# Kernel tuning notes

Hardware: AMD Instinct MI355X
Metric: run time of the kernel (lower is better)

## Reference

```python
import jax, jax.numpy as jnp
import numpy as np

B, N, K, D = 4096, 64, 48, 64   # batch, n_features, n_bins, d_embedding
F = N * D                        # flattened embedding dim
E, H, O = 8, 1024, 512           # experts, expert hidden, expert out
T, TH = 2, 256                   # tasks, tower hidden


def setup_inputs() -> dict:
    key = jax.random.key(0)
    ks = jax.random.split(key, 10)
    # PLE buffers from uniform bins linspace(0,1,K+1): w = 1/width, b = -edge/width
    edges = jnp.linspace(0.0, 1.0, K + 1)
    width = jnp.diff(edges)
    w = 1.0 / width                      # (K,)
    b = -edges[:-1] / width              # (K,)
    ple_weight = jnp.broadcast_to(w, (N, K)).astype(jnp.float32)
    ple_bias = jnp.broadcast_to(b, (N, K)).astype(jnp.float32)
    s = lambda fan_in: fan_in ** -0.5
    return {
        "x": jax.random.uniform(ks[0], (B, N), jnp.float32),
        "ple_weight": ple_weight,
        "ple_bias": ple_bias,
        "emb_W": jax.random.normal(ks[1], (N, K, D), jnp.float32) * s(K),
        "emb_b": jax.random.normal(ks[2], (N, D), jnp.float32) * s(K),
        "gate_W": jax.random.normal(ks[3], (F, E), jnp.float32) * s(F),
        "gate_b": jnp.zeros((E,), jnp.float32),
        "e_W1": jax.random.normal(ks[4], (E, F, H), jnp.float32) * s(F),
        "e_b1": jnp.zeros((E, H), jnp.float32),
        "e_W2": jax.random.normal(ks[5], (E, H, O), jnp.float32) * s(H),
        "e_b2": jnp.zeros((E, O), jnp.float32),
        "tw1": jax.random.normal(ks[6], (T, O, TH), jnp.float32) * s(O),
        "tb1": jnp.zeros((T, TH), jnp.float32),
        "tw2": jax.random.normal(ks[7], (T, TH, 1), jnp.float32) * s(TH),
        "tb2": jnp.zeros((T, 1), jnp.float32),
        "top_k": 2,
    }


def reference(x, ple_weight, ple_bias, emb_W, emb_b, gate_W, gate_b,
              e_W1, e_b1, e_W2, e_b2, tw1, tb1, tw2, tb2, top_k):
    # --- Piecewise Linear Encoding: (B, N) -> (B, N, K) ---
    enc = ple_bias + ple_weight * x[..., None]
    enc = jnp.concatenate([
        jnp.minimum(enc[..., :1], 1.0),
        jnp.clip(enc[..., 1:-1], 0.0, 1.0),
        jnp.maximum(enc[..., -1:], 0.0),
    ], axis=-1)
    # --- PLE embeddings via NLinear + ReLU: (B, N, K) -> (B, N, D) ---
    emb = jax.nn.relu(jnp.einsum("bnk,nkd->bnd", enc, emb_W) + emb_b)
    flat = emb.reshape(emb.shape[0], -1)                 # (B, F)
    # --- Sparse MoE gating (softmax + top-k renormalized) ---
    probs = jax.nn.softmax(flat @ gate_W + gate_b, axis=-1)   # (B, E)
    topv, topi = jax.lax.top_k(probs, top_k)
    topv = topv / jnp.sum(topv, axis=-1, keepdims=True)
    gates = jnp.zeros_like(probs).at[jnp.arange(probs.shape[0])[:, None], topi].set(topv)
    # --- Experts (computed densely, gated combine) ---
    h = jax.nn.relu(jnp.einsum("bf,efh->beh", flat, e_W1) + e_b1)   # (B, E, H)
    eo = jnp.einsum("beh,eho->beo", h, e_W2) + e_b2                 # (B, E, O)
    moe = jnp.einsum("be,beo->bo", gates, eo)                       # (B, O)
    # --- Task towers: per-task MLP -> scalar ---
    th = jax.nn.relu(jnp.einsum("bo,tos->bts", moe, tw1) + tb1)     # (B, T, TH)
    out = (jnp.einsum("bts,tsu->btu", th, tw2) + tb2)[..., 0]       # (B, T)
    return out
```

## Files before the change

### kernel.cpp

```cpp
#include <hip/hip_runtime.h>
#include <cstdint>

#define B_ 4096
#define N_ 64
#define K_ 48
#define D_ 64
#define F_ 4096
#define E_ 8
#define H_ 1024
#define O_ 512
#define T_ 2
#define TH_ 256
#define NSLOT (B_ * 2)

#define MAXT1 72

typedef float f32x4 __attribute__((ext_vector_type(4)));
typedef __bf16 bf16x8 __attribute__((ext_vector_type(8)));

__device__ __forceinline__ unsigned short f2bf(float f) {
    union { float f; unsigned int u; } v; v.f = f;
    unsigned int u = v.u;
    u += 0x7FFFu + ((u >> 16) & 1u);
    return (unsigned short)(u >> 16);
}

__device__ __forceinline__ void gload_lds16(const void* gptr, void* lptr) {
    auto* g = reinterpret_cast<const __attribute__((address_space(1))) unsigned int*>(
        reinterpret_cast<uintptr_t>(gptr));
    auto* l = reinterpret_cast<__attribute__((address_space(3))) unsigned int*>(
        reinterpret_cast<uintptr_t>(lptr));
    __builtin_amdgcn_global_load_lds(g, l, 16, 0, 0);
}

__global__ __launch_bounds__(64) void prefix_kernel(
    const float* __restrict__ embW, const float* __restrict__ embB,
    float* __restrict__ P)
{
    int n = blockIdx.x;
    int lane = threadIdx.x;
    float acc = embB[n * D_ + lane];
    const float* wsrc = embW + (size_t)n * K_ * D_ + lane;
    float* dst = P + (size_t)n * K_ * D_ + lane;
    #pragma unroll 8
    for (int k = 0; k < K_; ++k) {
        dst[k * D_] = acc;
        acc += wsrc[k * D_];
    }
}

__global__ __launch_bounds__(256) void ple_embed_kernel(
    const float* __restrict__ x, const float* __restrict__ plw,
    const float* __restrict__ plb, const float* __restrict__ embW,
    const float* __restrict__ P, const float* __restrict__ gateW,
    unsigned short* __restrict__ flat_bf, float* __restrict__ logits)
{
    __shared__ float gpart[4][E_];
    int b = blockIdx.x;
    int tid = threadIdx.x, lane = tid & 63, w = tid >> 6;

    float xl = x[b * N_ + lane];
    float gp[E_];
    #pragma unroll
    for (int e = 0; e < E_; ++e) gp[e] = 0.0f;

    #pragma unroll 4
    for (int i = 0; i < 16; ++i) {
        int n = w * 16 + i;
        float xn = __shfl(xl, n);
        const float* pw = plw + n * K_;
        const float* pb = plb + n * K_;
        float t = fmaf(pw[0], xn, pb[0]);
        int j = (int)t;
        j = max(0, min(K_ - 1, j));
        float f = fminf(fmaxf(fmaf(pw[j], xn, pb[j]), 0.0f), 1.0f);
        size_t base = ((size_t)n * K_ + j) * D_ + lane;
        float emb = fmaxf(fmaf(f, embW[base], P[base]), 0.0f);
        flat_bf[(size_t)b * F_ + n * D_ + lane] = f2bf(emb);

        const float4* gw4 = (const float4*)(gateW + (size_t)(n * D_ + lane) * E_);
        float4 g0 = gw4[0], g1 = gw4[1];
        gp[0] = fmaf(emb, g0.x, gp[0]);
        gp[1] = fmaf(emb, g0.y, gp[1]);
        gp[2] = fmaf(emb, g0.z, gp[2]);
        gp[3] = fmaf(emb, g0.w, gp[3]);
        gp[4] = fmaf(emb, g1.x, gp[4]);
        gp[5] = fmaf(emb, g1.y, gp[5]);
        gp[6] = fmaf(emb, g1.z, gp[6]);
        gp[7] = fmaf(emb, g1.w, gp[7]);
    }

    #pragma unroll
    for (int off = 32; off > 0; off >>= 1) {
        #pragma unroll
        for (int e = 0; e < E_; ++e) gp[e] += __shfl_down(gp[e], off);
    }
    if (lane == 0) {
        #pragma unroll
        for (int e = 0; e < E_; ++e) gpart[w][e] = gp[e];
    }
    __syncthreads();
    if (tid < E_)
        logits[b * E_ + tid] =
            gpart[0][tid] + gpart[1][tid] + gpart[2][tid] + gpart[3][tid];
}

__global__ __launch_bounds__(256) void gate_top2_kernel(
    const float* __restrict__ logits, const float* __restrict__ gate_b,
    int* __restrict__ topi, float* __restrict__ topg, int* __restrict__ counts)
{
    int b = blockIdx.x * 256 + threadIdx.x;
    int lane = threadIdx.x & 63;
    float l[E_];
    #pragma unroll
    for (int e = 0; e < E_; ++e) l[e] = logits[b * E_ + e] + gate_b[e];
    int e1 = 0; float v1 = l[0];
    #pragma unroll
    for (int e = 1; e < E_; ++e) if (l[e] > v1) { v1 = l[e]; e1 = e; }
    int e2 = -1; float v2 = -1e30f;
    #pragma unroll
    for (int e = 0; e < E_; ++e) if (e != e1 && l[e] > v2) { v2 = l[e]; e2 = e; }
    float ex = expf(v2 - v1);
    float g1 = 1.0f / (1.0f + ex);
    float g2 = ex / (1.0f + ex);
    topi[b * 2] = e1; topi[b * 2 + 1] = e2;
    topg[b * 2] = g1; topg[b * 2 + 1] = g2;
    #pragma unroll
    for (int e = 0; e < E_; ++e) {
        unsigned long long m1 = __ballot(e1 == e);
        unsigned long long m2 = __ballot(e2 == e);
        if (lane == 0) {
            int c = __popcll(m1) + __popcll(m2);
            if (c) atomicAdd(&counts[e], c);
        }
    }
}

__global__ void scan_kernel(const int* __restrict__ counts, int* __restrict__ offsets,
                            int* __restrict__ tiles1, int* __restrict__ ntiles) {
    int e = threadIdx.x;
    if (e >= E_) return;
    int c[E_];
    #pragma unroll
    for (int i = 0; i < E_; ++i) c[i] = counts[i];
    int off = 0, tb = 0, tot = 0, ttot = 0;
    #pragma unroll
    for (int i = 0; i < E_; ++i) {
        int t = (c[i] + 127) >> 7;
        if (i < e) { off += c[i]; tb += t; }
        tot += c[i]; ttot += t;
    }
    offsets[e] = off;
    if (e == 0) { offsets[E_] = tot; ntiles[0] = ttot; }
    int nt = (c[e] + 127) >> 7;
    for (int tr = 0; tr < nt; ++tr) tiles1[tb + tr] = (e << 16) | tr;
}

__global__ __launch_bounds__(256) void scatter_kernel(
    const int* __restrict__ topi, const float* __restrict__ topg,
    const int* __restrict__ offsets, int* __restrict__ cursors,
    int* __restrict__ rows, float* __restrict__ gatev, int* __restrict__ slots)
{
    int b = blockIdx.x * 256 + threadIdx.x;
    int lane = threadIdx.x & 63;
    #pragma unroll
    for (int j = 0; j < 2; ++j) {
        int e = topi[b * 2 + j];
        float g = topg[b * 2 + j];
        #pragma unroll
        for (int ex = 0; ex < E_; ++ex) {
            unsigned long long m = __ballot(e == ex);
            if (e == ex) {
                int leader = __builtin_ctzll(m);
                int base = 0;
                if (lane == leader) base = atomicAdd(&cursors[ex], __popcll(m));
                base = __shfl(base, leader);
                int pos = base + __popcll(m & ((1ull << lane) - 1ull));
                int slot = offsets[ex] + pos;
                rows[slot] = b;
                gatev[slot] = g;
                slots[b * 2 + j] = slot;
            }
        }
    }
}

__global__ __launch_bounds__(256) void wfrag_kernel(
    const float* __restrict__ in, unsigned short* __restrict__ out, int R, int C)
{
    __shared__ float tile[64][65];
    int e = blockIdx.z;
    int rb = blockIdx.x, cb = blockIdx.y;
    const float* src = in + (size_t)e * R * C + (size_t)(rb * 64) * C + cb * 64;
    int lane = threadIdx.x & 63, w = threadIdx.x >> 6;
    #pragma unroll
    for (int i = 0; i < 16; ++i) {
        int r = w * 16 + i;
        tile[r][lane] = src[(size_t)r * C + lane];
    }
    __syncthreads();
    int NB = C >> 4, KB = R >> 5;
    #pragma unroll
    for (int it = 0; it < 2; ++it) {
        int t = threadIdx.x + it * 256;
        int n0r = t >> 7, k0r = (t >> 6) & 1, ln = t & 63;
        int q = ln >> 4, nl = ln & 15;
        unsigned short v[8];
        #pragma unroll
        for (int j = 0; j < 8; ++j)
            v[j] = f2bf(tile[k0r * 32 + q * 8 + j][n0r * 16 + nl]);
        size_t didx = (((size_t)e * NB + cb * 4 + n0r) * KB + rb * 2 + k0r) * 512
                      + (size_t)ln * 8;
        uint4 pk;
        pk.x = v[0] | ((unsigned)v[1] << 16);
        pk.y = v[2] | ((unsigned)v[3] << 16);
        pk.z = v[4] | ((unsigned)v[5] << 16);
        pk.w = v[6] | ((unsigned)v[7] << 16);
        *(uint4*)&out[didx] = pk;
    }
}

__global__ __launch_bounds__(256) void fc1_kernel(
    const unsigned short* __restrict__ Abf,
    const unsigned short* __restrict__ Wf,
    const float* __restrict__ bias,
    const int* __restrict__ rows, const int* __restrict__ offsets,
    const int* __restrict__ tiles1, const int* __restrict__ ntiles,
    unsigned short* __restrict__ Hbf)
{
    int bid = blockIdx.x;
    int tlow = bid & 7;
    int rest = bid >> 3;
    int cn   = rest & 15;
    int tile = (rest >> 4) * 8 + tlow;
    if (tile >= ntiles[0]) return;
    int te = tiles1[tile];
    int e = te >> 16, tr = te & 0xffff;
    int m0 = offsets[e], mEnd = offsets[e + 1];
    int Me = mEnd - m0;

    __shared__ alignas(16) unsigned short As[2][128 * 64];

    int tid = threadIdx.x, lane = tid & 63, wv = tid >> 6;
    int lr = lane >> 3;
    int cg = (lane & 7) ^ lr;

    const unsigned short* aptr[4];
    #pragma unroll
    for (int i = 0; i < 4; ++i) {
        int rowA = (wv * 4 + i) * 8 + lr;
        int slot = min(m0 + tr * 128 + rowA, mEnd - 1);
        aptr[i] = Abf + (size_t)rows[slot] * F_ + cg * 8;
    }

    int wvM = wv >> 1, wvN = wv & 1;
    int m16 = lane & 15, q = lane >> 4;

    const unsigned short* bbase[2];
    #pragma unroll
    for (int nt = 0; nt < 2; ++nt) {
        int n0 = cn * 4 + wvN * 2 + nt;
        bbase[nt] = Wf + (((size_t)e * (H_ / 16) + n0) * (F_ / 32)) * 512
                    + (size_t)lane * 8;
    }

    f32x4 zero = {0.f, 0.f, 0.f, 0.f};
    f32x4 acc[4][2];
    #pragma unroll
    for (int i = 0; i < 4; ++i)
        #pragma unroll
        for (int j = 0; j < 2; ++j) acc[i][j] = zero;

#define FC_STAGE(BUF, KK) do {                                              \
    _Pragma("unroll")                                                       \
    for (int i_ = 0; i_ < 4; ++i_)                                          \
        gload_lds16(aptr[i_] + (KK), &As[BUF][(wv * 4 + i_) * 512]);        \
} while (0)

#define FC_LOADB(DST, KK) do {                                              \
    _Pragma("unroll")                                                       \
    for (int nt_ = 0; nt_ < 2; ++nt_)                                       \
        _Pragma("unroll")                                                   \
        for (int ks_ = 0; ks_ < 2; ++ks_)                                   \
            DST[nt_][ks_] = *(const bf16x8*)(bbase[nt_]                     \
                + (size_t)(KK) * 16 + ks_ * 512);                           \
} while (0)

#define FC_COMPUTE(BUF, BF) do {                                            \
    _Pragma("unroll")                                                       \
    for (int ks_ = 0; ks_ < 2; ++ks_) {                                     \
        bf16x8 af_[4];                                                      \
        _Pragma("unroll")                                                   \
        for (int mt_ = 0; mt_ < 4; ++mt_) {                                 \
            int m_ = wvM * 64 + mt_ * 16 + m16;                             \
            int pos_ = (ks_ * 4 + q) ^ (m_ & 7);                            \
            af_[mt_] = *(const bf16x8*)&As[BUF][m_ * 64 + pos_ * 8];        \
        }                                                                   \
        _Pragma("unroll")                                                   \
        for (int mt_ = 0; mt_ < 4; ++mt_)                                   \
            _Pragma("unroll")                                               \
            for (int nt_ = 0; nt_ < 2; ++nt_)                               \
                acc[mt_][nt_] = __builtin_amdgcn_mfma_f32_16x16x32_bf16(    \
                    af_[mt_], BF[nt_][ks_], acc[mt_][nt_], 0, 0, 0);        \
    }                                                                       \
} while (0)

#define FC_WAIT8() asm volatile("s_waitcnt vmcnt(8)" ::: "memory")
#define FC_WAIT0() asm volatile("s_waitcnt vmcnt(0)" ::: "memory")
#define FC_BAR()   __builtin_amdgcn_s_barrier()

    bf16x8 bA[2][2], bB[2][2];
    FC_STAGE(0, 0);
    FC_LOADB(bA, 0);

    for (int k0 = 0; k0 < F_; k0 += 128) {
        FC_STAGE(1, k0 + 64);
        FC_LOADB(bB, k0 + 64);
        FC_WAIT8();
        FC_BAR();
        FC_COMPUTE(0, bA);
        FC_BAR();

        if (k0 + 128 < F_) {
            FC_STAGE(0, k0 + 128);
            FC_LOADB(bA, k0 + 128);
            FC_WAIT8();
        } else {
            FC_WAIT0();
        }
        FC_BAR();
        FC_COMPUTE(1, bB);
        FC_BAR();
    }

    #pragma unroll
    for (int nt = 0; nt < 2; ++nt) {
        int col = cn * 64 + wvN * 32 + nt * 16 + m16;
        float bv = bias[e * H_ + col];
        #pragma unroll
        for (int mt = 0; mt < 4; ++mt) {
            int rbase = tr * 128 + wvM * 64 + mt * 16 + q * 4;
            #pragma unroll
            for (int r = 0; r < 4; ++r) {
                int rr = rbase + r;
                if (rr < Me) {
                    float v = fmaxf(acc[mt][nt][r] + bv, 0.0f);
                    Hbf[(size_t)(m0 + rr) * H_ + col] = f2bf(v);
                }
            }
        }
    }
}

__global__ __launch_bounds__(256) void fc2_kernel(
    const unsigned short* __restrict__ Hbf,
    const unsigned short* __restrict__ Wf,
    const float* __restrict__ bias,
    const int* __restrict__ offsets, const int* __restrict__ tiles1,
    const int* __restrict__ ntiles, float* __restrict__ eo)
{
    int bid = blockIdx.x;
    int tlow = bid & 7;
    int rest = bid >> 3;
    int cn   = rest & 7;
    int tile = (rest >> 3) * 8 + tlow;
    if (tile >= ntiles[0]) return;
    int te = tiles1[tile];
    int e = te >> 16, tr = te & 0xffff;
    int m0 = offsets[e], mEnd = offsets[e + 1];
    int Me = mEnd - m0;

    __shared__ alignas(16) unsigned short As[2][128 * 64];

    int tid = threadIdx.x, lane = tid & 63, wv = tid >> 6;
    int lr = lane >> 3;
    int cg = (lane & 7) ^ lr;

    const unsigned short* aptr[4];
    #pragma unroll
    for (int i = 0; i < 4; ++i) {
        int rowA = (wv * 4 + i) * 8 + lr;
        int slot = min(m0 + tr * 128 + rowA, mEnd - 1);
        aptr[i] = Hbf + (size_t)slot * H_ + cg * 8;
    }

    int wvM = wv >> 1, wvN = wv & 1;
    int m16 = lane & 15, q = lane >> 4;

    const unsigned short* bbase[2];
    #pragma unroll
    for (int nt = 0; nt < 2; ++nt) {
        int n0 = cn * 4 + wvN * 2 + nt;
        bbase[nt] = Wf + (((size_t)e * (O_ / 16) + n0) * (H_ / 32)) * 512
                    + (size_t)lane * 8;
    }

    f32x4 zero = {0.f, 0.f, 0.f, 0.f};
    f32x4 acc[4][2];
    #pragma unroll
    for (int i = 0; i < 4; ++i)
        #pragma unroll
        for (int j = 0; j < 2; ++j) acc[i][j] = zero;

    bf16x8 bA[2][2], bB[2][2];
    FC_STAGE(0, 0);
    FC_LOADB(bA, 0);

    for (int k0 = 0; k0 < H_; k0 += 128) {
        FC_STAGE(1, k0 + 64);
        FC_LOADB(bB, k0 + 64);
        FC_WAIT8();
        FC_BAR();
        FC_COMPUTE(0, bA);
        FC_BAR();

        if (k0 + 128 < H_) {
            FC_STAGE(0, k0 + 128);
            FC_LOADB(bA, k0 + 128);
            FC_WAIT8();
        } else {
            FC_WAIT0();
        }
        FC_BAR();
        FC_COMPUTE(1, bB);
        FC_BAR();
    }

    #pragma unroll
    for (int nt = 0; nt < 2; ++nt) {
        int col = cn * 64 + wvN * 32 + nt * 16 + m16;
        float bv = bias[e * O_ + col];
        #pragma unroll
        for (int mt = 0; mt < 4; ++mt) {
            int rbase = tr * 128 + wvM * 64 + mt * 16 + q * 4;
            #pragma unroll
            for (int r = 0; r < 4; ++r) {
                int rr = rbase + r;
                if (rr < Me) {
                    eo[(size_t)(m0 + rr) * O_ + col] = acc[mt][nt][r] + bv;
                }
            }
        }
    }
}

#undef FC_STAGE
#undef FC_LOADB
#undef FC_COMPUTE
#undef FC_WAIT8
#undef FC_WAIT0
#undef FC_BAR

__global__ __launch_bounds__(256) void moe_combine_kernel(
    const float* __restrict__ eo, const int* __restrict__ slots,
    const float* __restrict__ gatev, float* __restrict__ moe)
{
    int gid = blockIdx.x * 256 + threadIdx.x;
    int b = gid >> 7;
    int c = (gid & 127) * 4;
    int s0 = slots[b * 2];
    int s1 = slots[b * 2 + 1];
    float g0 = gatev[s0];
    float g1 = gatev[s1];
    float4 v0 = *(const float4*)&eo[(size_t)s0 * O_ + c];
    float4 v1 = *(const float4*)&eo[(size_t)s1 * O_ + c];
    float4 r;
    r.x = g0 * v0.x + g1 * v1.x;
    r.y = g0 * v0.y + g1 * v1.y;
    r.z = g0 * v0.z + g1 * v1.z;
    r.w = g0 * v0.w + g1 * v1.w;
    *(float4*)&moe[(size_t)b * O_ + c] = r;
}

__global__ __launch_bounds__(256) void tower_kernel(
    const float* __restrict__ moe, const float* __restrict__ tw1,
    const float* __restrict__ tb1, const float* __restrict__ tw2,
    const float* __restrict__ tb2, float* __restrict__ out)
{
    __shared__ float ms[8 * O_];
    __shared__ float red[16][4];
    int b0 = blockIdx.x * 8;
    int tid = threadIdx.x, lane = tid & 63, wv = tid >> 6;
    for (int idx = tid; idx < 8 * O_; idx += 256)
        ms[idx] = moe[(size_t)b0 * O_ + idx];
    __syncthreads();

    int s = tid;
    float a0[8], a1[8];
    float bv0 = tb1[s], bv1 = tb1[TH_ + s];
    #pragma unroll
    for (int i = 0; i < 8; ++i) { a0[i] = bv0; a1[i] = bv1; }

    for (int o = 0; o < O_; o += 4) {
        float w0[4], w1[4];
        #pragma unroll
        for (int u = 0; u < 4; ++u) {
            w0[u] = tw1[(size_t)(o + u) * TH_ + s];
            w1[u] = tw1[(size_t)(O_ + o + u) * TH_ + s];
        }
        #pragma unroll
        for (int i = 0; i < 8; ++i) {
            float4 mv = *(const float4*)&ms[i * O_ + o];
            a0[i] = fmaf(mv.x, w0[0], a0[i]);
            a0[i] = fmaf(mv.y, w0[1], a0[i]);
            a0[i] = fmaf(mv.z, w0[2], a0[i]);
            a0[i] = fmaf(mv.w, w0[3], a0[i]);
            a1[i] = fmaf(mv.x, w1[0], a1[i]);
            a1[i] = fmaf(mv.y, w1[1], a1[i]);
            a1[i] = fmaf(mv.z, w1[2], a1[i]);
            a1[i] = fmaf(mv.w, w1[3], a1[i]);
        }
    }

    float w2a = tw2[s], w2b = tw2[TH_ + s];
    #pragma unroll
    for (int i = 0; i < 8; ++i) {
        float p0 = fmaxf(a0[i], 0.0f) * w2a;
        float p1 = fmaxf(a1[i], 0.0f) * w2b;
        #pragma unroll
        for (int off = 32; off > 0; off >>= 1) {
            p0 += __shfl_down(p0, off);
            p1 += __shfl_down(p1, off);
        }
        if (lane == 0) { red[i * 2 + 0][wv] = p0; red[i * 2 + 1][wv] = p1; }
    }
    __syncthreads();
    if (tid < 16) {
        int i = tid >> 1, t = tid & 1;
        float v = red[tid][0] + red[tid][1] + red[tid][2] + red[tid][3] + tb2[t];
        out[(size_t)(b0 + i) * T_ + t] = v;
    }
}

extern "C" void kernel_launch(void* const* d_in, const int* in_sizes, int n_in,
                              void* d_out, int out_size, void* d_ws, size_t ws_size,
                              hipStream_t stream)
{
    const float* x     = (const float*)d_in[0];
    const float* plw   = (const float*)d_in[1];
    const float* plb   = (const float*)d_in[2];
    const float* embW  = (const float*)d_in[3];
    const float* embB  = (const float*)d_in[4];
    const float* gateW = (const float*)d_in[5];
    const float* gateB = (const float*)d_in[6];
    const float* eW1   = (const float*)d_in[7];
    const float* eB1   = (const float*)d_in[8];
    const float* eW2   = (const float*)d_in[9];
    const float* eB2   = (const float*)d_in[10];
    const float* tw1   = (const float*)d_in[11];
    const float* tb1   = (const float*)d_in[12];
    const float* tw2   = (const float*)d_in[13];
    const float* tb2   = (const float*)d_in[14];
    float* out = (float*)d_out;

    char* w = (char*)d_ws;
    auto alloc = [&](size_t bytes) {
        char* p = w; w += (bytes + 255) & ~(size_t)255; return p;
    };
    unsigned short* flat_bf = (unsigned short*)alloc((size_t)B_ * F_ * 2);
    unsigned short* W1f     = (unsigned short*)alloc((size_t)E_ * H_ * F_ * 2);
    unsigned short* W2f     = (unsigned short*)alloc((size_t)E_ * O_ * H_ * 2);
    unsigned short* Hbf     = (unsigned short*)alloc((size_t)NSLOT * H_ * 2);
    float* eo      = (float*)alloc((size_t)NSLOT * O_ * 4);
    float* Ppre    = (float*)alloc((size_t)N_ * K_ * D_ * 4);
    float* logits  = (float*)alloc((size_t)B_ * E_ * 4);
    float* moe     = (float*)alloc((size_t)B_ * O_ * 4);
    int*   topi    = (int*)alloc((size_t)B_ * 2 * 4);
    float* topg    = (float*)alloc((size_t)B_ * 2 * 4);
    int*   rows    = (int*)alloc((size_t)NSLOT * 4);
    float* gatev   = (float*)alloc((size_t)NSLOT * 4);
    int*   slots   = (int*)alloc((size_t)B_ * 2 * 4);
    int*   counts  = (int*)alloc(E_ * 4);
    int*   offsets = (int*)alloc((E_ + 1) * 4);
    int*   cursors = (int*)alloc(E_ * 4);
    int*   tiles1  = (int*)alloc(MAXT1 * 4);
    int*   ntiles  = (int*)alloc(2 * 4);

    hipMemsetAsync(counts, 0, E_ * 4, stream);
    hipMemsetAsync(cursors, 0, E_ * 4, stream);

    prefix_kernel<<<N_, 64, 0, stream>>>(embW, embB, Ppre);
    ple_embed_kernel<<<B_, 256, 0, stream>>>(x, plw, plb, embW, Ppre, gateW,
                                             flat_bf, logits);
    wfrag_kernel<<<dim3(F_ / 64, H_ / 64, E_), 256, 0, stream>>>(eW1, W1f, F_, H_);
    wfrag_kernel<<<dim3(H_ / 64, O_ / 64, E_), 256, 0, stream>>>(eW2, W2f, H_, O_);
    gate_top2_kernel<<<B_ / 256, 256, 0, stream>>>(logits, gateB, topi, topg, counts);
    scan_kernel<<<1, 64, 0, stream>>>(counts, offsets, tiles1, ntiles);
    scatter_kernel<<<B_ / 256, 256, 0, stream>>>(topi, topg, offsets, cursors,
                                                 rows, gatev, slots);
    fc1_kernel<<<MAXT1 * 16, 256, 0, stream>>>(flat_bf, W1f, eB1, rows, offsets,
                                               tiles1, ntiles, Hbf);
    fc2_kernel<<<MAXT1 * 8, 256, 0, stream>>>(Hbf, W2f, eB2, offsets,
                                              tiles1, ntiles, eo);
    moe_combine_kernel<<<(B_ * O_ / 4) / 256, 256, 0, stream>>>(eo, slots, gatev, moe);
    tower_kernel<<<B_ / 8, 256, 0, stream>>>(moe, tw1, tb1, tw2, tb2, out);
}
```

Before: 525.1 us.

## Retile expert GEMM waves to own their A rows and drop block barriers

Both expert GEMM kernels change their wave layout from 2x2 (each wave 64 rows x 32 cols) to 4x1 (each wave 32 rows x 64 cols). Each wave now reads from LDS only the A rows it staged itself, so the four s_barrier calls per iteration are replaced by wave-local vmcnt/lgkmcnt waits and sched_barrier fences. The aim is to remove block-wide synchronisation stalls and let waves run out of lockstep. In exchange, each wave loads twice as many B fragments from global memory and holds more B registers, which raises L2 traffic and register pressure.

```diff
diff --git a/kernel.cpp b/kernel.cpp
--- a/kernel.cpp
+++ b/kernel.cpp
@@ -253,23 +253,22 @@
         aptr[i] = Abf + (size_t)rows[slot] * F_ + cg * 8;
     }
 
-    int wvM = wv >> 1, wvN = wv & 1;
     int m16 = lane & 15, q = lane >> 4;
 
-    const unsigned short* bbase[2];
-    #pragma unroll
-    for (int nt = 0; nt < 2; ++nt) {
-        int n0 = cn * 4 + wvN * 2 + nt;
+    const unsigned short* bbase[4];
+    #pragma unroll
+    for (int nt = 0; nt < 4; ++nt) {
+        int n0 = cn * 4 + nt;
         bbase[nt] = Wf + (((size_t)e * (H_ / 16) + n0) * (F_ / 32)) * 512
                     + (size_t)lane * 8;
     }
 
     f32x4 zero = {0.f, 0.f, 0.f, 0.f};
-    f32x4 acc[4][2];
-    #pragma unroll
-    for (int i = 0; i < 4; ++i)
-        #pragma unroll
-        for (int j = 0; j < 2; ++j) acc[i][j] = zero;
+    f32x4 acc[2][4];
+    #pragma unroll
+    for (int i = 0; i < 2; ++i)
+        #pragma unroll
+        for (int j = 0; j < 4; ++j) acc[i][j] = zero;
 
 #define FC_STAGE(BUF, KK) do {                                              \
     _Pragma("unroll")                                                       \
@@ -279,7 +278,7 @@
 
 #define FC_LOADB(DST, KK) do {                                              \
     _Pragma("unroll")                                                       \
-    for (int nt_ = 0; nt_ < 2; ++nt_)                                       \
+    for (int nt_ = 0; nt_ < 4; ++nt_)                                       \
         _Pragma("unroll")                                                   \
         for (int ks_ = 0; ks_ < 2; ++ks_)                                   \
             DST[nt_][ks_] = *(const bf16x8*)(bbase[nt_]                     \
@@ -289,57 +288,61 @@
 #define FC_COMPUTE(BUF, BF) do {                                            \
     _Pragma("unroll")                                                       \
     for (int ks_ = 0; ks_ < 2; ++ks_) {                                     \
-        bf16x8 af_[4];                                                      \
+        bf16x8 af_[2];                                                      \
         _Pragma("unroll")                                                   \
-        for (int mt_ = 0; mt_ < 4; ++mt_) {                                 \
-            int m_ = wvM * 64 + mt_ * 16 + m16;                             \
+        for (int mt_ = 0; mt_ < 2; ++mt_) {                                 \
+            int m_ = wv * 32 + mt_ * 16 + m16;                              \
             int pos_ = (ks_ * 4 + q) ^ (m_ & 7);                            \
             af_[mt_] = *(const bf16x8*)&As[BUF][m_ * 64 + pos_ * 8];        \
         }                                                                   \
         _Pragma("unroll")                                                   \
-        for (int mt_ = 0; mt_ < 4; ++mt_)                                   \
+        for (int mt_ = 0; mt_ < 2; ++mt_)                                   \
             _Pragma("unroll")                                               \
-            for (int nt_ = 0; nt_ < 2; ++nt_)                               \
+            for (int nt_ = 0; nt_ < 4; ++nt_)                               \
                 acc[mt_][nt_] = __builtin_amdgcn_mfma_f32_16x16x32_bf16(    \
                     af_[mt_], BF[nt_][ks_], acc[mt_][nt_], 0, 0, 0);        \
     }                                                                       \
 } while (0)
 
-#define FC_WAIT8() asm volatile("s_waitcnt vmcnt(8)" ::: "memory")
-#define FC_WAIT0() asm volatile("s_waitcnt vmcnt(0)" ::: "memory")
-#define FC_BAR()   __builtin_amdgcn_s_barrier()
-
-    bf16x8 bA[2][2], bB[2][2];
+#define FC_WAIT12() do {                                                    \
+    asm volatile("s_waitcnt vmcnt(12)" ::: "memory");                       \
+    __builtin_amdgcn_sched_barrier(0);                                      \
+} while (0)
+#define FC_WAIT0() do {                                                     \
+    asm volatile("s_waitcnt vmcnt(0)" ::: "memory");                        \
+    __builtin_amdgcn_sched_barrier(0);                                      \
+} while (0)
+#define FC_WAITL() asm volatile("s_waitcnt lgkmcnt(0)" ::: "memory")
+
+    bf16x8 bA[4][2], bB[4][2];
     FC_STAGE(0, 0);
     FC_LOADB(bA, 0);
 
     for (int k0 = 0; k0 < F_; k0 += 128) {
+        FC_WAITL();
         FC_STAGE(1, k0 + 64);
         FC_LOADB(bB, k0 + 64);
-        FC_WAIT8();
-        FC_BAR();
+        FC_WAIT12();
         FC_COMPUTE(0, bA);
-        FC_BAR();
 
         if (k0 + 128 < F_) {
+            FC_WAITL();
             FC_STAGE(0, k0 + 128);
             FC_LOADB(bA, k0 + 128);
-            FC_WAIT8();
+            FC_WAIT12();
         } else {
             FC_WAIT0();
         }
-        FC_BAR();
         FC_COMPUTE(1, bB);
-        FC_BAR();
-    }
-
-    #pragma unroll
-    for (int nt = 0; nt < 2; ++nt) {
-        int col = cn * 64 + wvN * 32 + nt * 16 + m16;
+    }
+
+    #pragma unroll
+    for (int nt = 0; nt < 4; ++nt) {
+        int col = cn * 64 + nt * 16 + m16;
         float bv = bias[e * H_ + col];
         #pragma unroll
-        for (int mt = 0; mt < 4; ++mt) {
-            int rbase = tr * 128 + wvM * 64 + mt * 16 + q * 4;
+        for (int mt = 0; mt < 2; ++mt) {
+            int rbase = tr * 128 + wv * 32 + mt * 16 + q * 4;
             #pragma unroll
             for (int r = 0; r < 4; ++r) {
                 int rr = rbase + r;
@@ -384,55 +387,52 @@
         aptr[i] = Hbf + (size_t)slot * H_ + cg * 8;
     }
 
-    int wvM = wv >> 1, wvN = wv & 1;
     int m16 = lane & 15, q = lane >> 4;
 
-    const unsigned short* bbase[2];
-    #pragma unroll
-    for (int nt = 0; nt < 2; ++nt) {
-        int n0 = cn * 4 + wvN * 2 + nt;
+    const unsigned short* bbase[4];
+    #pragma unroll
+    for (int nt = 0; nt < 4; ++nt) {
+        int n0 = cn * 4 + nt;
         bbase[nt] = Wf + (((size_t)e * (O_ / 16) + n0) * (H_ / 32)) * 512
                     + (size_t)lane * 8;
     }
 
     f32x4 zero = {0.f, 0.f, 0.f, 0.f};
-    f32x4 acc[4][2];
-    #pragma unroll
-    for (int i = 0; i < 4; ++i)
-        #pragma unroll
-        for (int j = 0; j < 2; ++j) acc[i][j] = zero;
-
-    bf16x8 bA[2][2], bB[2][2];
+    f32x4 acc[2][4];
+    #pragma unroll
+    for (int i = 0; i < 2; ++i)
+        #pragma unroll
+        for (int j = 0; j < 4; ++j) acc[i][j] = zero;
+
+    bf16x8 bA[4][2], bB[4][2];
     FC_STAGE(0, 0);
     FC_LOADB(bA, 0);
 
     for (int k0 = 0; k0 < H_; k0 += 128) {
+        FC_WAITL();
         FC_STAGE(1, k0 + 64);
         FC_LOADB(bB, k0 + 64);
-        FC_WAIT8();
-        FC_BAR();
+        FC_WAIT12();
         FC_COMPUTE(0, bA);
-        FC_BAR();
 
         if (k0 + 128 < H_) {
+            FC_WAITL();
             FC_STAGE(0, k0 + 128);
             FC_LOADB(bA, k0 + 128);
-            FC_WAIT8();
+            FC_WAIT12();
         } else {
             FC_WAIT0();
         }
-        FC_BAR();
         FC_COMPUTE(1, bB);
-        FC_BAR();
-    }
-
-    #pragma unroll
-    for (int nt = 0; nt < 2; ++nt) {
-        int col = cn * 64 + wvN * 32 + nt * 16 + m16;
+    }
+
+    #pragma unroll
+    for (int nt = 0; nt < 4; ++nt) {
+        int col = cn * 64 + nt * 16 + m16;
         float bv = bias[e * O_ + col];
         #pragma unroll
-        for (int mt = 0; mt < 4; ++mt) {
-            int rbase = tr * 128 + wvM * 64 + mt * 16 + q * 4;
+        for (int mt = 0; mt < 2; ++mt) {
+            int rbase = tr * 128 + wv * 32 + mt * 16 + q * 4;
             #pragma unroll
             for (int r = 0; r < 4; ++r) {
                 int rr = rbase + r;
@@ -447,9 +447,9 @@
 #undef FC_STAGE
 #undef FC_LOADB
 #undef FC_COMPUTE
-#undef FC_WAIT8
+#undef FC_WAIT12
 #undef FC_WAIT0
-#undef FC_BAR
+#undef FC_WAITL
 
 __global__ __launch_bounds__(256) void moe_combine_kernel(
     const float* __restrict__ eo, const int* __restrict__ slots,
```

Result: slower. 556.8 us (+6.0%).
